# Performance work log

Measured on AMD Instinct MI355X. Metric: run time of the kernel, lower is better.

The kernel has to match this reference:

```python
import jax, jax.numpy as jnp
import numpy as np

DIM = 384
HEADS = 8
RATES = (0.5, 0.75)  # sparse_rates
EPS = 1e-12  # torch F.normalize default eps


def _dwconv3x3(x, w):
    # depthwise 3x3, padding=1; w: [3*dim, 1, 3, 3]
    return jax.lax.conv_general_dilated(
        x, w, window_strides=(1, 1), padding=((1, 1), (1, 1)),
        feature_group_count=w.shape[0],
        dimension_numbers=('NCHW', 'OIHW', 'NCHW'))


def setup_inputs() -> dict:
    key = jax.random.key(0)
    ks = jax.random.split(key, 5)
    dim = DIM
    x = jax.random.normal(ks[0], (4, dim, 128, 128), jnp.float32)
    qkv_w = jax.random.normal(ks[1], (3 * dim, dim), jnp.float32) * 0.05   # 1x1 conv
    dw_w = jax.random.normal(ks[2], (3 * dim, 1, 3, 3), jnp.float32) * 0.1  # depthwise 3x3
    proj_w = jax.random.normal(ks[3], (dim, dim), jnp.float32) * 0.05       # 1x1 conv
    temperature = jnp.ones((HEADS, 1, 1), jnp.float32)
    attns = jnp.full((len(RATES),), 0.2, jnp.float32)
    return {"x": x, "qkv_w": qkv_w, "dw_w": dw_w, "proj_w": proj_w,
            "temperature": temperature, "attns": attns}


def reference(x, qkv_w, dw_w, proj_w, temperature, attns) -> jnp.ndarray:
    b, c, h, w = x.shape
    qkv = jnp.einsum('bchw,oc->bohw', x, qkv_w)  # 1x1 conv, no bias
    qkv = _dwconv3x3(qkv, dw_w)
    q, k, v = jnp.split(qkv, 3, axis=1)

    def heads(t):  # b (head c) h w -> b head c (h w)
        return t.reshape(b, HEADS, c // HEADS, h * w)

    q, k, v = heads(q), heads(k), heads(v)
    q = q / jnp.maximum(jnp.linalg.norm(q, axis=-1, keepdims=True), EPS)
    k = k / jnp.maximum(jnp.linalg.norm(k, axis=-1, keepdims=True), EPS)
    C = q.shape[2]
    attn = jnp.einsum('bhcn,bhdn->bhcd', q, k) * temperature  # [b, head, C, C]

    out = jnp.zeros_like(v)  # [b, head, C, HW]
    for i, rate in enumerate(RATES):
        kk = int(C * rate)
        _, idx = jax.lax.top_k(attn, kk)                      # [b, head, C, kk]
        mask = jax.nn.one_hot(idx, C, dtype=attn.dtype).sum(-2) > 0  # scatter 1s
        attn = jnp.where(mask, attn, -jnp.inf)
        attn = jax.nn.softmax(attn, axis=-1)  # NOTE: original reuses softmaxed attn next iter
        out = out + jnp.einsum('bhcd,bhdn->bhcn', attn, v) * attns[i]

    out = out.reshape(b, c, h, w)  # b head c (hw) -> b (head c) h w
    return jnp.einsum('bchw,oc->bohw', out, proj_w)
```

## Files before the change

### kernel.cpp

```cpp
#include <hip/hip_runtime.h>
#include <math.h>

#define HW     16384
#define WIDTH  128
#define CDIM   384
#define QKVC   1152
#define HEADS  8
#define CH     48
#define NSPLIT 32
#define GK     384

typedef unsigned short u16;
typedef short bf16x8 __attribute__((ext_vector_type(8)));
typedef float f32x4 __attribute__((ext_vector_type(4)));

__device__ __forceinline__ void split2(float x, u16& h, u16& l) {
    union { float f; unsigned u; } a, b, c;
    a.f = x;
    unsigned hu = (a.u + 0x7fffu + ((a.u >> 16) & 1u)) & 0xffff0000u;
    b.u = hu;
    h = (u16)(hu >> 16);
    c.f = x - b.f;
    l = (u16)((c.u + 0x7fffu + ((c.u >> 16) & 1u)) >> 16);
}

__device__ __forceinline__ void gload16(const void* g, void* l) {
    __builtin_amdgcn_global_load_lds((const __attribute__((address_space(1))) unsigned int*)g,
                                     (__attribute__((address_space(3))) unsigned int*)l, 16, 0, 0);
}

__global__ __launch_bounds__(512)
void mfma_gemm(const u16* __restrict__ Ah, const u16* __restrict__ Al,
               const u16* __restrict__ Bh, const u16* __restrict__ Bl,
               float* __restrict__ C, int nmb,
               long abs_, long bbs, long cbs)
{
    extern __shared__ char smem[];
    const int tot = gridDim.x * gridDim.y;
    const int per = tot >> 3;
    const int fl  = blockIdx.x + gridDim.x * blockIdx.y;
    const int f2  = (fl & 7) * per + (fl >> 3);
    const int nblk = f2 / nmb, mblk = f2 % nmb;
    const int b = blockIdx.z;
    Ah += (long)b * abs_; Al += (long)b * abs_;
    Bh += (long)b * bbs;  Bl += (long)b * bbs;
    C  += (long)b * cbs;
    const int m0 = mblk * 128, n0 = nblk * 256;

    const int tid  = threadIdx.x;
    const int wave = tid >> 6, lane = tid & 63;
    const int lr = lane & 15, lg = lane >> 4;
    const int wm = wave >> 2, wn = wave & 3;
    const int wb = wave * 1024;

    const int sr  = tid >> 2;
    const int kxs = (tid & 3) ^ ((sr >> 1) & 3);

    f32x4 acc[4][4];
#pragma unroll
    for (int i = 0; i < 4; ++i)
#pragma unroll
        for (int j = 0; j < 4; ++j) acc[i][j] = (f32x4){0.f, 0.f, 0.f, 0.f};

#define STAGE(bufsel, kt) do {                                                     \
        char* L = smem + (bufsel) * 49152;                                         \
        const long ko = (long)(kt) * 32 + kxs * 8;                                 \
        gload16(Ah + (long)(m0 + sr) * GK + ko,        L + wb);                    \
        gload16(Al + (long)(m0 + sr) * GK + ko,        L + 8192  + wb);            \
        gload16(Bh + (long)(n0 + sr) * GK + ko,        L + 16384 + wb);            \
        gload16(Bh + (long)(n0 + 128 + sr) * GK + ko,  L + 24576 + wb);            \
        gload16(Bl + (long)(n0 + sr) * GK + ko,        L + 32768 + wb);            \
        gload16(Bl + (long)(n0 + 128 + sr) * GK + ko,  L + 40960 + wb);            \
    } while (0)

    STAGE(0, 0);
    __syncthreads();
    int cur = 0;
    for (int kt = 0; kt < GK / 32; ++kt) {
        if (kt + 1 < GK / 32) STAGE(cur ^ 1, kt + 1);
        const char* L = smem + cur * 49152;
        bf16x8 af[4][2], bf[4][2];
#pragma unroll
        for (int mi = 0; mi < 4; ++mi) {
            int r = wm * 64 + mi * 16 + lr;
            int off = r * 64 + (((lg ^ (r >> 1)) & 3) << 4);
            af[mi][0] = *(const bf16x8*)(L + off);
            af[mi][1] = *(const bf16x8*)(L + 8192 + off);
        }
#pragma unroll
        for (int ni = 0; ni < 4; ++ni) {
            int r = wn * 64 + ni * 16 + lr;
            int off = r * 64 + (((lg ^ (r >> 1)) & 3) << 4);
            bf[ni][0] = *(const bf16x8*)(L + 16384 + off);
            bf[ni][1] = *(const bf16x8*)(L + 32768 + off);
        }
        __builtin_amdgcn_s_setprio(1);
#pragma unroll
        for (int mi = 0; mi < 4; ++mi)
#pragma unroll
            for (int ni = 0; ni < 4; ++ni) {
                acc[mi][ni] = __builtin_amdgcn_mfma_f32_16x16x32_bf16(af[mi][0], bf[ni][0], acc[mi][ni], 0, 0, 0);
                acc[mi][ni] = __builtin_amdgcn_mfma_f32_16x16x32_bf16(af[mi][0], bf[ni][1], acc[mi][ni], 0, 0, 0);
                acc[mi][ni] = __builtin_amdgcn_mfma_f32_16x16x32_bf16(af[mi][1], bf[ni][0], acc[mi][ni], 0, 0, 0);
            }
        __builtin_amdgcn_s_setprio(0);
        __syncthreads();
        cur ^= 1;
    }
#undef STAGE

#pragma unroll
    for (int mi = 0; mi < 4; ++mi)
#pragma unroll
        for (int ni = 0; ni < 4; ++ni) {
            int row = m0 + wm * 64 + mi * 16 + lg * 4;
            int col = n0 + wn * 64 + ni * 16 + lr;
            float* cp = C + (long)row * HW + col;
            cp[0]          = acc[mi][ni][0];
            cp[(long)HW]   = acc[mi][ni][1];
            cp[2L * HW]    = acc[mi][ni][2];
            cp[3L * HW]    = acc[mi][ni][3];
        }
}

__global__ __launch_bounds__(256)
void convT_kernel(const float* __restrict__ in, u16* __restrict__ oh, u16* __restrict__ ol,
                  long ibs, long obs)
{
    const int b = blockIdx.z;
    in += (long)b * ibs; oh += (long)b * obs; ol += (long)b * obs;
    __shared__ float t[32][33];
    const int p0 = blockIdx.x * 32, c0 = blockIdx.y * 32;
    const int ty = threadIdx.x >> 5, tx = threadIdx.x & 31;
#pragma unroll
    for (int it = 0; it < 4; ++it) {
        int c = ty + it * 8;
        t[c][tx] = in[(long)(c0 + c) * HW + p0 + tx];
    }
    __syncthreads();
#pragma unroll
    for (int it = 0; it < 4; ++it) {
        int p = ty + it * 8;
        u16 h, l;
        split2(t[tx][p], h, l);
        long o = (long)(p0 + p) * CDIM + c0 + tx;
        oh[o] = h; ol[o] = l;
    }
}

__global__ __launch_bounds__(256)
void convA_kernel(const float* __restrict__ in, u16* __restrict__ oh, u16* __restrict__ ol, int n)
{
    int i = blockIdx.x * 256 + threadIdx.x;
    if (i < n) split2(in[i], oh[i], ol[i]);
}

__global__ __launch_bounds__(256)
void dwconv_kernel(const float* __restrict__ in, const float* __restrict__ w,
                   float* __restrict__ out)
{
    const long base = (long)blockIdx.y * QKVC * HW;
    const int idx = blockIdx.x * 256 + threadIdx.x;
    const int ch = idx >> 11;
    const int wi = idx & 2047;
    const int y = wi >> 4, x0 = (wi & 15) * 8;
    const float* wp = w + ch * 9;
    const float* ip = in + base + (long)ch * HW;
    float o[8] = {0.f, 0.f, 0.f, 0.f, 0.f, 0.f, 0.f, 0.f};
#pragma unroll
    for (int dy = -1; dy <= 1; ++dy) {
        int yy = y + dy;
        if ((unsigned)yy >= 128u) continue;
        const float* rp = ip + yy * WIDTH + x0;
        float4 a  = *(const float4*)rp;
        float4 bq = *(const float4*)(rp + 4);
        float v[10] = { (x0 > 0) ? rp[-1] : 0.f,
                        a.x, a.y, a.z, a.w, bq.x, bq.y, bq.z, bq.w,
                        (x0 < 120) ? rp[8] : 0.f };
        float w0 = wp[(dy + 1) * 3], w1 = wp[(dy + 1) * 3 + 1], w2 = wp[(dy + 1) * 3 + 2];
#pragma unroll
        for (int j = 0; j < 8; ++j)
            o[j] = fmaf(w0, v[j], fmaf(w1, v[j + 1], fmaf(w2, v[j + 2], o[j])));
    }
    float* op = out + base + (long)ch * HW + y * WIDTH + x0;
    *(float4*)op       = (float4){o[0], o[1], o[2], o[3]};
    *(float4*)(op + 4) = (float4){o[4], o[5], o[6], o[7]};
}

__global__ __launch_bounds__(256)
void attn_partial_kernel(const float* __restrict__ dw, float* __restrict__ part,
                         float* __restrict__ part2, long ps, long p2s)
{
    const int split = blockIdx.x, h = blockIdx.y, b = blockIdx.z;
    const int n0 = split * (HW / NSPLIT);
    const float* qbase = dw + ((long)b * QKVC + h * CH) * HW;
    const float* kbase = dw + ((long)b * QKVC + CDIM + h * CH) * HW;
    __shared__ float qs[64][CH];
    __shared__ float ks[64][CH];
    const int tid = threadIdx.x;
    const int tr = tid >> 4, tc = tid & 15;
    const int c0 = tr * 3, d0 = tc * 3;
    float acc[3][3] = {{0.f}};
    float qss[3] = {0.f, 0.f, 0.f}, kss[3] = {0.f, 0.f, 0.f};
    const int cA = tid >> 4;
    const int nq = (tid & 15) * 4;
    for (int ns = 0; ns < HW / NSPLIT; ns += 64) {
        __syncthreads();
#pragma unroll
        for (int t = 0; t < 3; ++t) {
            int c = cA + t * 16;
            float4 qv = *(const float4*)(qbase + (long)c * HW + n0 + ns + nq);
            float4 kv = *(const float4*)(kbase + (long)c * HW + n0 + ns + nq);
            qs[nq + 0][c] = qv.x; qs[nq + 1][c] = qv.y;
            qs[nq + 2][c] = qv.z; qs[nq + 3][c] = qv.w;
            ks[nq + 0][c] = kv.x; ks[nq + 1][c] = kv.y;
            ks[nq + 2][c] = kv.z; ks[nq + 3][c] = kv.w;
            qss[t] += qv.x * qv.x + qv.y * qv.y + qv.z * qv.z + qv.w * qv.w;
            kss[t] += kv.x * kv.x + kv.y * kv.y + kv.z * kv.z + kv.w * kv.w;
        }
        __syncthreads();
#pragma unroll 8
        for (int n = 0; n < 64; ++n) {
            float q0 = qs[n][c0], q1 = qs[n][c0 + 1], q2 = qs[n][c0 + 2];
            float k0 = ks[n][d0], k1 = ks[n][d0 + 1], k2 = ks[n][d0 + 2];
            acc[0][0] = fmaf(q0, k0, acc[0][0]); acc[0][1] = fmaf(q0, k1, acc[0][1]); acc[0][2] = fmaf(q0, k2, acc[0][2]);
            acc[1][0] = fmaf(q1, k0, acc[1][0]); acc[1][1] = fmaf(q1, k1, acc[1][1]); acc[1][2] = fmaf(q1, k2, acc[1][2]);
            acc[2][0] = fmaf(q2, k0, acc[2][0]); acc[2][1] = fmaf(q2, k1, acc[2][1]); acc[2][2] = fmaf(q2, k2, acc[2][2]);
        }
    }
#pragma unroll
    for (int m = 1; m < 16; m <<= 1) {
#pragma unroll
        for (int t = 0; t < 3; ++t) {
            qss[t] += __shfl_xor(qss[t], m);
            kss[t] += __shfl_xor(kss[t], m);
        }
    }
    if ((tid & 15) == 0) {
        float* p2 = part2 + (long)b * p2s + ((long)h * NSPLIT + split) * 96;
#pragma unroll
        for (int t = 0; t < 3; ++t) {
            p2[cA + t * 16]      = qss[t];
            p2[48 + cA + t * 16] = kss[t];
        }
    }
    float* po = part + (long)b * ps + ((long)h * NSPLIT + split) * (CH * CH);
#pragma unroll
    for (int i = 0; i < 3; ++i)
#pragma unroll
        for (int j = 0; j < 3; ++j)
            po[(c0 + i) * CH + d0 + j] = acc[i][j];
}

__global__ __launch_bounds__(256)
void attn_reduce_kernel(const float* __restrict__ part, const float* __restrict__ part2,
                        const float* __restrict__ temp, float* __restrict__ attn,
                        long ps, long p2s, long as_)
{
    const int seg = blockIdx.x, h = blockIdx.y, b = blockIdx.z;
    const float* pp = part + (long)b * ps + (long)h * NSPLIT * (CH * CH);
    const float* p2 = part2 + (long)b * p2s + (long)h * NSPLIT * 96;
    __shared__ float sinv[96];
    if (threadIdx.x < 96) {
        float s = 0.f;
        for (int sp = 0; sp < NSPLIT; ++sp) s += p2[sp * 96 + threadIdx.x];
        sinv[threadIdx.x] = 1.f / fmaxf(sqrtf(s), 1e-12f);
    }
    __syncthreads();
    const float t = temp[h];
    const int idx = seg * 256 + threadIdx.x;
    const int c = idx / CH, d = idx % CH;
    float s = 0.f;
    for (int sp = 0; sp < NSPLIT; ++sp) s += pp[sp * (CH * CH) + idx];
    attn[(long)b * as_ + (long)h * (CH * CH) + idx] = s * sinv[c] * sinv[48 + d] * t;
}

__global__ __launch_bounds__(256)
void maskw_kernel(const float* __restrict__ attn, const float* __restrict__ attns,
                  float* __restrict__ W, long as_, long ws_)
{
    const int h = blockIdx.y, b = blockIdx.z;
    const int wave = threadIdx.x >> 6, lane = threadIdx.x & 63;
    const int r = blockIdx.x * 4 + wave;
    const float* ap = attn + (long)b * as_ + (long)h * (CH * CH) + (long)r * CH;
    float a = (lane < CH) ? ap[lane] : -3.4e38f;

    int rank = 0;
#pragma unroll
    for (int j = 0; j < CH; ++j) {
        float aj = __shfl(a, j);
        rank += (aj > a) || (aj == a && j < lane);
    }
    const bool keep = (lane < CH) && (rank < 24);
    float m = keep ? a : -3.4e38f;
#pragma unroll
    for (int o = 32; o > 0; o >>= 1) m = fmaxf(m, __shfl_xor(m, o));
    float e = keep ? expf(a - m) : 0.f;
    float s = e;
#pragma unroll
    for (int o = 32; o > 0; o >>= 1) s += __shfl_xor(s, o);
    const float A1 = e / s;

    int rank2 = 0;
#pragma unroll
    for (int j = 0; j < CH; ++j) {
        float aj = __shfl(A1, j);
        rank2 += (aj > A1) || (aj == A1 && j < lane);
    }
    const bool keep2 = (lane < CH) && (rank2 < 36);
    float m2 = keep2 ? A1 : -3.4e38f;
#pragma unroll
    for (int o = 32; o > 0; o >>= 1) m2 = fmaxf(m2, __shfl_xor(m2, o));
    float e2 = keep2 ? expf(A1 - m2) : 0.f;
    float s2 = e2;
#pragma unroll
    for (int o = 32; o > 0; o >>= 1) s2 += __shfl_xor(s2, o);

    if (lane < CH)
        W[(long)b * ws_ + (long)h * (CH * CH) + (long)r * CH + lane] =
            attns[0] * A1 + attns[1] * (e2 / s2);
}

__global__ __launch_bounds__(256)
void mbuild_kernel(const float* __restrict__ P, const float* __restrict__ W,
                   u16* __restrict__ Mh, u16* __restrict__ Ml, long ws_, long ms)
{
    const int b = blockIdx.y;
    const int idx = blockIdx.x * 256 + threadIdx.x;
    const int o = idx / CDIM, col = idx % CDIM;
    const int h = col / CH, d = col % CH;
    const float* wp = W + (long)b * ws_ + (long)h * (CH * CH) + d;
    const float* pp = P + (long)o * CDIM + h * CH;
    float s = 0.f;
#pragma unroll
    for (int c = 0; c < CH; ++c) s = fmaf(pp[c], wp[c * CH], s);
    u16 hh, ll;
    split2(s, hh, ll);
    Mh[(long)b * ms + idx] = hh;
    Ml[(long)b * ms + idx] = ll;
}

extern "C" void kernel_launch(void* const* d_in, const int* in_sizes, int n_in,
                              void* d_out, int out_size, void* d_ws, size_t ws_size,
                              hipStream_t stream)
{
    const float* x      = (const float*)d_in[0];
    const float* qkv_w  = (const float*)d_in[1];
    const float* dw_w   = (const float*)d_in[2];
    const float* proj_w = (const float*)d_in[3];
    const float* temp   = (const float*)d_in[4];
    const float* attns  = (const float*)d_in[5];
    float* out = (float*)d_out;

    const size_t perbB = (size_t)QKVC * HW * 4;
    auto need = [&](int nb) -> size_t {
        return (size_t)nb * 2 * perbB + 4u * QKVC * CDIM + 4096;
    };
    int NB = 4;
    while (NB > 1 && need(NB) > ws_size) NB >>= 1;

    const long fstride = (long)(perbB / 4);
    const long ustride = (long)(perbB / 2);

    const size_t PART_B  = 27u << 20;
    const size_t PART2_B = (29u << 20) + (512u << 10);
    const size_t ATT_B   = 30u << 20;
    const size_t WM_B    = 31u << 20;
    const size_t MH_B    = 32u << 20;
    const size_t ML_B    = 33u << 20;

    char* buf1 = (char*)d_ws;
    char* buf2 = buf1 + (size_t)NB * perbB;
    u16* Ah = (u16*)(buf2 + (size_t)NB * perbB);
    u16* Al = Ah + (size_t)QKVC * CDIM;

    convA_kernel<<<dim3((QKVC * CDIM + 255) / 256), 256, 0, stream>>>(qkv_w, Ah, Al, QKVC * CDIM);

    for (int b0 = 0; b0 < 4; b0 += NB) {
        const int nb = NB;
        float* pre = (float*)buf1;
        float* dwb = (float*)buf2;
        u16* xt_h = (u16*)buf2;                u16* xt_l = xt_h + (size_t)HW * CDIM;
        u16* vt_h = (u16*)buf1;                u16* vt_l = vt_h + (size_t)HW * CDIM;
        float* part  = (float*)(buf1 + PART_B);
        float* part2 = (float*)(buf1 + PART2_B);
        float* attn  = (float*)(buf1 + ATT_B);
        float* Wm    = (float*)(buf1 + WM_B);
        u16* Mh = (u16*)(buf1 + MH_B);
        u16* Ml = (u16*)(buf1 + ML_B);

        convT_kernel<<<dim3(HW / 32, CDIM / 32, nb), 256, 0, stream>>>(
            x + (size_t)b0 * CDIM * HW, xt_h, xt_l, (long)CDIM * HW, ustride);
        mfma_gemm<<<dim3(HW / 256, QKVC / 128, nb), 512, 98304, stream>>>(
            Ah, Al, xt_h, xt_l, pre, QKVC / 128, 0L, ustride, fstride);
        dwconv_kernel<<<dim3(QKVC * HW / 8 / 256, nb), 256, 0, stream>>>(pre, dw_w, dwb);
        attn_partial_kernel<<<dim3(NSPLIT, HEADS, nb), 256, 0, stream>>>(dwb, part, part2,
                                                                         fstride, fstride);
        attn_reduce_kernel<<<dim3(9, HEADS, nb), 256, 0, stream>>>(part, part2, temp, attn,
                                                                   fstride, fstride, fstride);
        maskw_kernel<<<dim3(12, HEADS, nb), 256, 0, stream>>>(attn, attns, Wm, fstride, fstride);
        mbuild_kernel<<<dim3(CDIM * CDIM / 256, nb), 256, 0, stream>>>(proj_w, Wm, Mh, Ml,
                                                                       fstride, ustride);
        convT_kernel<<<dim3(HW / 32, CDIM / 32, nb), 256, 0, stream>>>(
            dwb + (size_t)2 * CDIM * HW, vt_h, vt_l, fstride, ustride);
        mfma_gemm<<<dim3(HW / 256, CDIM / 128, nb), 512, 98304, stream>>>(
            Mh, Ml, vt_h, vt_l, out + (size_t)b0 * CDIM * HW, CDIM / 128,
            ustride, ustride, (long)CDIM * HW);
    }
}
```

Before: 698.5 us.

## Deepen GEMM LDS pipeline with explicit vmcnt waits and vectorize transpose stores

```diff
diff --git a/kernel.cpp b/kernel.cpp
--- a/kernel.cpp
+++ b/kernel.cpp
@@ -63,21 +63,24 @@
         for (int j = 0; j < 4; ++j) acc[i][j] = (f32x4){0.f, 0.f, 0.f, 0.f};
 
 #define STAGE(bufsel, kt) do {                                                     \
-        char* L = smem + (bufsel) * 49152;                                         \
+        char* LL = smem + (bufsel) * 49152;                                        \
         const long ko = (long)(kt) * 32 + kxs * 8;                                 \
-        gload16(Ah + (long)(m0 + sr) * GK + ko,        L + wb);                    \
-        gload16(Al + (long)(m0 + sr) * GK + ko,        L + 8192  + wb);            \
-        gload16(Bh + (long)(n0 + sr) * GK + ko,        L + 16384 + wb);            \
-        gload16(Bh + (long)(n0 + 128 + sr) * GK + ko,  L + 24576 + wb);            \
-        gload16(Bl + (long)(n0 + sr) * GK + ko,        L + 32768 + wb);            \
-        gload16(Bl + (long)(n0 + 128 + sr) * GK + ko,  L + 40960 + wb);            \
+        gload16(Ah + (long)(m0 + sr) * GK + ko,        LL + wb);                   \
+        gload16(Al + (long)(m0 + sr) * GK + ko,        LL + 8192  + wb);           \
+        gload16(Bh + (long)(n0 + sr) * GK + ko,        LL + 16384 + wb);           \
+        gload16(Bh + (long)(n0 + 128 + sr) * GK + ko,  LL + 24576 + wb);           \
+        gload16(Bl + (long)(n0 + sr) * GK + ko,        LL + 32768 + wb);           \
+        gload16(Bl + (long)(n0 + 128 + sr) * GK + ko,  LL + 40960 + wb);           \
     } while (0)
 
     STAGE(0, 0);
-    __syncthreads();
+    STAGE(1, 1);
     int cur = 0;
-    for (int kt = 0; kt < GK / 32; ++kt) {
-        if (kt + 1 < GK / 32) STAGE(cur ^ 1, kt + 1);
+    for (int kt = 0; kt < 12; ++kt) {
+        if (kt < 11) asm volatile("s_waitcnt vmcnt(6)" ::: "memory");
+        else         asm volatile("s_waitcnt vmcnt(0)" ::: "memory");
+        __builtin_amdgcn_s_barrier();
+
         const char* L = smem + cur * 49152;
         bf16x8 af[4][2], bf[4][2];
 #pragma unroll
@@ -94,6 +97,11 @@
             bf[ni][0] = *(const bf16x8*)(L + 16384 + off);
             bf[ni][1] = *(const bf16x8*)(L + 32768 + off);
         }
+        asm volatile("s_waitcnt lgkmcnt(0)" ::: "memory");
+        __builtin_amdgcn_sched_barrier(0);
+        __builtin_amdgcn_s_barrier();
+        if (kt < 10) STAGE(cur, kt + 2);
+
         __builtin_amdgcn_s_setprio(1);
 #pragma unroll
         for (int mi = 0; mi < 4; ++mi)
@@ -104,7 +112,6 @@
                 acc[mi][ni] = __builtin_amdgcn_mfma_f32_16x16x32_bf16(af[mi][1], bf[ni][0], acc[mi][ni], 0, 0, 0);
             }
         __builtin_amdgcn_s_setprio(0);
-        __syncthreads();
         cur ^= 1;
     }
 #undef STAGE
@@ -138,13 +145,17 @@
         t[c][tx] = in[(long)(c0 + c) * HW + p0 + tx];
     }
     __syncthreads();
-#pragma unroll
-    for (int it = 0; it < 4; ++it) {
-        int p = ty + it * 8;
-        u16 h, l;
-        split2(t[tx][p], h, l);
-        long o = (long)(p0 + p) * CDIM + c0 + tx;
-        oh[o] = h; ol[o] = l;
+    const int cp = threadIdx.x & 15;
+    const int py = threadIdx.x >> 4;
+#pragma unroll
+    for (int half = 0; half < 2; ++half) {
+        int p = py + half * 16;
+        u16 h0, l0, h1, l1;
+        split2(t[2 * cp][p], h0, l0);
+        split2(t[2 * cp + 1][p], h1, l1);
+        long o = (long)(p0 + p) * CDIM + c0 + 2 * cp;
+        *(ushort2*)&oh[o] = (ushort2){h0, h1};
+        *(ushort2*)&ol[o] = (ushort2){l0, l1};
     }
 }
 
```

Measured after the change: 696.9 us. About the same (-0.2%).
